# Performance work log

Hardware: AMD Instinct MI355X
Metric: run time of the kernel (lower is better)

Reference implementation:

```python
import jax
import jax.numpy as jnp
from jax import lax
import numpy as np

INPUT_SIZE = 2
COND_SIZE = 4
HIDDEN = 128
LATENT = 32
DEC_IN = INPUT_SIZE + LATENT + COND_SIZE + 1  # 39
DT = 0.05


def setup_inputs() -> dict:
    key = jax.random.key(0)
    ks = jax.random.split(key, 9)
    B = 8192
    s = 1.0 / np.sqrt(HIDDEN)  # PyTorch LSTM init scale
    z = jax.random.normal(ks[0], (B, LATENT), jnp.float32)
    condition = jax.random.normal(ks[1], (B, COND_SIZE), jnp.float32)
    start_point = jax.random.normal(ks[2], (B, INPUT_SIZE), jnp.float32)
    W_ih = jax.random.uniform(ks[3], (4 * HIDDEN, DEC_IN), jnp.float32, -s, s)
    W_hh = jax.random.uniform(ks[4], (4 * HIDDEN, HIDDEN), jnp.float32, -s, s)
    b_ih = jax.random.uniform(ks[5], (4 * HIDDEN,), jnp.float32, -s, s)
    b_hh = jax.random.uniform(ks[6], (4 * HIDDEN,), jnp.float32, -s, s)
    W_out = jax.random.uniform(ks[7], (INPUT_SIZE, HIDDEN), jnp.float32, -s, s)
    b_out = jax.random.uniform(ks[8], (INPUT_SIZE,), jnp.float32, -s, s)
    return {
        "z": z, "condition": condition, "start_point": start_point,
        "W_ih": W_ih, "W_hh": W_hh, "b_ih": b_ih, "b_hh": b_hh,
        "W_out": W_out, "b_out": b_out, "seq_len": 2048,
    }


def reference(z, condition, start_point, W_ih, W_hh, b_ih, b_hh, W_out, b_out, seq_len):
    B = z.shape[0]
    dt = jnp.full((B, 1), DT, dtype=z.dtype)  # constant delta_t per step
    # precompute the static part of the per-step input projection: [z, cond, dt]
    # columns of W_ih: [x(2) | z(32) | cond(4) | dt(1)]
    static_in = jnp.concatenate([z, condition, dt], axis=-1)  # [B, 37]
    static_proj = static_in @ W_ih[:, INPUT_SIZE:].T + b_ih + b_hh  # [B, 4H]
    W_ih_x = W_ih[:, :INPUT_SIZE]  # [4H, 2]

    def step(carry, _):
        x_t, h, c = carry
        gates = x_t @ W_ih_x.T + static_proj + h @ W_hh.T  # [B, 4H]
        i, f, g, o = jnp.split(gates, 4, axis=-1)
        i = jax.nn.sigmoid(i)
        f = jax.nn.sigmoid(f)
        g = jnp.tanh(g)
        o = jax.nn.sigmoid(o)
        c = f * c + i * g
        h = o * jnp.tanh(c)
        x_next = h @ W_out.T + b_out  # [B, input_size]
        return (x_next, h, c), x_next

    h0 = jnp.zeros((B, HIDDEN), z.dtype)
    c0 = jnp.zeros((B, HIDDEN), z.dtype)
    _, ys = lax.scan(step, (start_point, h0, c0), None, length=seq_len)
    return jnp.transpose(ys, (1, 0, 2))  # [B, seq_len, input_size]
```

## Files before the change

### kernel.cpp

```cpp
#include <hip/hip_runtime.h>

typedef short bf16x8 __attribute__((ext_vector_type(8)));
typedef float f32x4 __attribute__((ext_vector_type(4)));

#define LOG2E 1.44269504088896340736f

__device__ __forceinline__ unsigned short f2bf(float x) {
    unsigned u = __builtin_bit_cast(unsigned, x);
    return (unsigned short)((u + 0x7fffu + ((u >> 16) & 1u)) >> 16);
}

__global__ __launch_bounds__(512, 4)
void lstm_persist(const float* __restrict__ zP, const float* __restrict__ condP,
                  const float* __restrict__ startP, const float* __restrict__ WihP,
                  const float* __restrict__ WhhP, const float* __restrict__ bihP,
                  const float* __restrict__ bhhP, const float* __restrict__ WoutP,
                  const float* __restrict__ boutP, float* __restrict__ outP)
{
    __shared__ unsigned short hist[8 * 16 * 128];
    char* const lds = (char*)hist;

    const int tid  = threadIdx.x;
    const int wave = tid >> 6;
    const int lane = tid & 63;
    const int lo   = lane & 15;
    const int gq   = lane >> 4;
    const int r0   = blockIdx.x * 16;
    const int hid0 = wave * 16;

    const float K2 = 2.0f * LOG2E;
    const float ss[4] = { -LOG2E, -LOG2E, 2.0f * LOG2E, -LOG2E };

    float wxs0[4], wxs1[4], bias[4];
    bf16x8 bfrag[4][4];
    #pragma unroll
    for (int s = 0; s < 4; ++s) {
        const int col = s * 128 + hid0 + lo;
        const float wx0 = WihP[col * 39 + 0];
        const float wx1 = WihP[col * 39 + 1];
        wxs0[s] = ss[s] * wx0;
        wxs1[s] = ss[s] * wx1;
        bias[s] = bihP[col] + bhhP[col];
        #pragma unroll
        for (int kt = 0; kt < 4; ++kt) {
            bf16x8 f;
            #pragma unroll
            for (int j = 0; j < 8; ++j) {
                const int k = kt * 32 + gq * 8 + j;
                const float w = WhhP[col * 128 + k]
                              + wx0 * WoutP[k] + wx1 * WoutP[128 + k];
                f[j] = (short)f2bf(ss[s] * w);
            }
            bfrag[s][kt] = f;
        }
    }

    bf16x8 wof[4];
    #pragma unroll
    for (int kt = 0; kt < 4; ++kt) {
        bf16x8 f;
        #pragma unroll
        for (int j = 0; j < 8; ++j) {
            const int k = kt * 32 + gq * 8 + j;
            f[j] = (lo < 2) ? (short)f2bf(WoutP[lo * 128 + k]) : (short)0;
        }
        wof[kt] = f;
    }
    const float bo = (lo < 2) ? boutP[lo] : 0.0f;

    f32x4 sp[4];
    #pragma unroll
    for (int s = 0; s < 4; ++s)
        #pragma unroll
        for (int rr = 0; rr < 4; ++rr)
            sp[s][rr] = bias[s];

    for (int j = 0; j < 32; ++j) {
        float w[4];
        #pragma unroll
        for (int s = 0; s < 4; ++s) w[s] = WihP[(s * 128 + hid0 + lo) * 39 + 2 + j];
        #pragma unroll
        for (int rr = 0; rr < 4; ++rr) {
            const int row = r0 + gq * 4 + rr;
            const float si = zP[row * 32 + j];
            #pragma unroll
            for (int s = 0; s < 4; ++s) sp[s][rr] += si * w[s];
        }
    }
    for (int j = 0; j < 4; ++j) {
        float w[4];
        #pragma unroll
        for (int s = 0; s < 4; ++s) w[s] = WihP[(s * 128 + hid0 + lo) * 39 + 34 + j];
        #pragma unroll
        for (int rr = 0; rr < 4; ++rr) {
            const int row = r0 + gq * 4 + rr;
            const float si = condP[row * 4 + j];
            #pragma unroll
            for (int s = 0; s < 4; ++s) sp[s][rr] += si * w[s];
        }
    }
    #pragma unroll
    for (int s = 0; s < 4; ++s) {
        const float w = 0.05f * WihP[(s * 128 + hid0 + lo) * 39 + 38];
        #pragma unroll
        for (int rr = 0; rr < 4; ++rr) sp[s][rr] = ss[s] * (sp[s][rr] + w);
    }

    int wroff[4];
    #pragma unroll
    for (int rr = 0; rr < 4; ++rr) {
        const int row = gq * 4 + rr;
        wroff[rr] = (row * 256 + (hid0 + lo) * 2) ^ ((row & 7) << 4);
    }
    int rdoff[4];
    #pragma unroll
    for (int kt = 0; kt < 4; ++kt)
        rdoff[kt] = (lo * 256 + kt * 64 + gq * 16) ^ ((lo & 7) << 4);

    f32x4 cst = f32x4{0.f, 0.f, 0.f, 0.f};

    auto tail = [&](f32x4 (&acc)[4], const int wbase) {
        float h[4];
        #pragma unroll
        for (int rr = 0; rr < 4; ++rr) {
            const float si = __builtin_amdgcn_rcpf(1.0f + __builtin_amdgcn_exp2f(acc[0][rr]));
            const float sf = __builtin_amdgcn_rcpf(1.0f + __builtin_amdgcn_exp2f(acc[1][rr]));
            const float rg = __builtin_amdgcn_rcpf(1.0f + __builtin_amdgcn_exp2f(acc[2][rr]));
            const float so = __builtin_amdgcn_rcpf(1.0f + __builtin_amdgcn_exp2f(acc[3][rr]));
            const float tg = __builtin_fmaf(rg, -2.0f, 1.0f);
            const float cn = __builtin_fmaf(sf, cst[rr], si * tg);
            cst[rr] = cn;
            const float rc = __builtin_amdgcn_rcpf(1.0f + __builtin_amdgcn_exp2f(cn * K2));
            const float tc = __builtin_fmaf(rc, -2.0f, 1.0f);
            h[rr] = so * tc;
        }
        unsigned p01, p23;
        asm("v_cvt_pk_bf16_f32 %0, %1, %2" : "=v"(p01) : "v"(h[0]), "v"(h[1]));
        asm("v_cvt_pk_bf16_f32 %0, %1, %2" : "=v"(p23) : "v"(h[2]), "v"(h[3]));
        *(unsigned short*)(lds + wbase + wroff[0]) = (unsigned short)(p01 & 0xffffu);
        *(unsigned short*)(lds + wbase + wroff[1]) = (unsigned short)(p01 >> 16);
        *(unsigned short*)(lds + wbase + wroff[2]) = (unsigned short)(p23 & 0xffffu);
        *(unsigned short*)(lds + wbase + wroff[3]) = (unsigned short)(p23 >> 16);
    };

    {
        f32x4 acc0[4];
        #pragma unroll
        for (int s = 0; s < 4; ++s) acc0[s] = sp[s];
        #pragma unroll
        for (int rr = 0; rr < 4; ++rr) {
            const int row = r0 + gq * 4 + rr;
            const float x0 = startP[row * 2 + 0];
            const float x1 = startP[row * 2 + 1];
            #pragma unroll
            for (int s = 0; s < 4; ++s)
                acc0[s][rr] += x0 * wxs0[s] + x1 * wxs1[s];
        }
        tail(acc0, 0);
    }
    #pragma unroll
    for (int s = 0; s < 4; ++s) {
        const float bx = wxs0[s] * boutP[0] + wxs1[s] * boutP[1];
        #pragma unroll
        for (int rr = 0; rr < 4; ++rr) sp[s][rr] += bx;
    }
    __syncthreads();

    #pragma unroll 1
    for (int t = 1; t < 2048; ++t) {
        const int rbase = ((t - 1) & 7) * 4096;
        const int wbase = (t & 7) * 4096;

        bf16x8 af[4];
        #pragma unroll
        for (int kt = 0; kt < 4; ++kt)
            af[kt] = __builtin_bit_cast(bf16x8, *(const f32x4*)(lds + rbase + rdoff[kt]));

        f32x4 acc[4];
        #pragma unroll
        for (int s = 0; s < 4; ++s) {
            f32x4 a = sp[s];
            #pragma unroll
            for (int kt = 0; kt < 4; ++kt)
                a = __builtin_amdgcn_mfma_f32_16x16x32_bf16(af[kt], bfrag[s][kt], a, 0, 0, 0);
            acc[s] = a;
        }
        tail(acc, wbase);
        __syncthreads();

        if ((t & 7) == 7) {
            f32x4 xacc = f32x4{0.f, 0.f, 0.f, 0.f};
            #pragma unroll
            for (int kt = 0; kt < 4; ++kt) {
                const bf16x8 a = __builtin_bit_cast(bf16x8,
                    *(const f32x4*)(lds + wave * 4096 + rdoff[kt]));
                xacc = __builtin_amdgcn_mfma_f32_16x16x32_bf16(a, wof[kt], xacc, 0, 0, 0);
            }
            const int tg = t - 7 + wave;
            if (lo < 2) {
                #pragma unroll
                for (int rr = 0; rr < 4; ++rr) {
                    const int row = gq * 4 + rr;
                    outP[(size_t)(r0 + row) * 4096 + tg * 2 + lo] = xacc[rr] + bo;
                }
            }
            __syncthreads();
        }
    }
}

extern "C" void kernel_launch(void* const* d_in, const int* in_sizes, int n_in,
                              void* d_out, int out_size, void* d_ws, size_t ws_size,
                              hipStream_t stream) {
    const float* z    = (const float*)d_in[0];
    const float* cond = (const float*)d_in[1];
    const float* strt = (const float*)d_in[2];
    const float* Wih  = (const float*)d_in[3];
    const float* Whh  = (const float*)d_in[4];
    const float* bih  = (const float*)d_in[5];
    const float* bhh  = (const float*)d_in[6];
    const float* Wout = (const float*)d_in[7];
    const float* bout = (const float*)d_in[8];
    float* out = (float*)d_out;

    hipLaunchKernelGGL(lstm_persist, dim3(512), dim3(512), 0, stream,
                       z, cond, strt, Wih, Whh, bih, bhh, Wout, bout, out);
}
```

Before: 3.130 ms.

## Double LDS history ring, drop extra barrier, merge gate reciprocals, stagger blocks

```diff
diff --git a/kernel.cpp b/kernel.cpp
--- a/kernel.cpp
+++ b/kernel.cpp
@@ -17,7 +17,7 @@
                   const float* __restrict__ bhhP, const float* __restrict__ WoutP,
                   const float* __restrict__ boutP, float* __restrict__ outP)
 {
-    __shared__ unsigned short hist[8 * 16 * 128];
+    __shared__ unsigned short hist[16 * 16 * 128];
     char* const lds = (char*)hist;
 
     const int tid  = threadIdx.x;
@@ -123,16 +123,20 @@
         float h[4];
         #pragma unroll
         for (int rr = 0; rr < 4; ++rr) {
-            const float si = __builtin_amdgcn_rcpf(1.0f + __builtin_amdgcn_exp2f(acc[0][rr]));
-            const float sf = __builtin_amdgcn_rcpf(1.0f + __builtin_amdgcn_exp2f(acc[1][rr]));
-            const float rg = __builtin_amdgcn_rcpf(1.0f + __builtin_amdgcn_exp2f(acc[2][rr]));
-            const float so = __builtin_amdgcn_rcpf(1.0f + __builtin_amdgcn_exp2f(acc[3][rr]));
-            const float tg = __builtin_fmaf(rg, -2.0f, 1.0f);
-            const float cn = __builtin_fmaf(sf, cst[rr], si * tg);
+            const float yi = __builtin_amdgcn_exp2f(__builtin_fminf(acc[0][rr], 40.f));
+            const float yf = __builtin_amdgcn_exp2f(__builtin_fminf(acc[1][rr], 40.f));
+            const float yg = __builtin_amdgcn_exp2f(__builtin_fminf(acc[2][rr], 40.f));
+            const float yo = __builtin_amdgcn_exp2f(__builtin_fminf(acc[3][rr], 40.f));
+            const float pf  = 1.0f + yf;
+            const float pig = (1.0f + yi) * (1.0f + yg);
+            const float r3  = __builtin_amdgcn_rcpf(pf * pig);
+            const float sf  = pig * r3;
+            const float ig  = (yg - 1.0f) * pf * r3;
+            const float cn  = __builtin_fmaf(sf, cst[rr], ig);
             cst[rr] = cn;
-            const float rc = __builtin_amdgcn_rcpf(1.0f + __builtin_amdgcn_exp2f(cn * K2));
-            const float tc = __builtin_fmaf(rc, -2.0f, 1.0f);
-            h[rr] = so * tc;
+            const float yc  = __builtin_amdgcn_exp2f(__builtin_fminf(cn * K2, 40.f));
+            const float roc = __builtin_amdgcn_rcpf((1.0f + yo) * (1.0f + yc));
+            h[rr] = (yc - 1.0f) * roc;
         }
         unsigned p01, p23;
         asm("v_cvt_pk_bf16_f32 %0, %1, %2" : "=v"(p01) : "v"(h[0]), "v"(h[1]));
@@ -166,37 +170,25 @@
     }
     __syncthreads();
 
+    if (blockIdx.x & 1) {
+        asm volatile("s_sleep 7\n s_sleep 7\n s_sleep 7\n s_sleep 7\n s_sleep 7");
+    }
+
     #pragma unroll 1
     for (int t = 1; t < 2048; ++t) {
-        const int rbase = ((t - 1) & 7) * 4096;
-        const int wbase = (t & 7) * 4096;
-
-        bf16x8 af[4];
-        #pragma unroll
-        for (int kt = 0; kt < 4; ++kt)
-            af[kt] = __builtin_bit_cast(bf16x8, *(const f32x4*)(lds + rbase + rdoff[kt]));
-
-        f32x4 acc[4];
-        #pragma unroll
-        for (int s = 0; s < 4; ++s) {
-            f32x4 a = sp[s];
-            #pragma unroll
-            for (int kt = 0; kt < 4; ++kt)
-                a = __builtin_amdgcn_mfma_f32_16x16x32_bf16(af[kt], bfrag[s][kt], a, 0, 0, 0);
-            acc[s] = a;
-        }
-        tail(acc, wbase);
-        __syncthreads();
-
-        if ((t & 7) == 7) {
+        const int rbase = ((t - 1) & 15) * 4096;
+        const int wbase = (t & 15) * 4096;
+
+        if ((t & 7) == 0) {
+            const int sbase = (wave + ((t - 8) & 15)) * 4096;
             f32x4 xacc = f32x4{0.f, 0.f, 0.f, 0.f};
             #pragma unroll
             for (int kt = 0; kt < 4; ++kt) {
                 const bf16x8 a = __builtin_bit_cast(bf16x8,
-                    *(const f32x4*)(lds + wave * 4096 + rdoff[kt]));
+                    *(const f32x4*)(lds + sbase + rdoff[kt]));
                 xacc = __builtin_amdgcn_mfma_f32_16x16x32_bf16(a, wof[kt], xacc, 0, 0, 0);
             }
-            const int tg = t - 7 + wave;
+            const int tg = t - 8 + wave;
             if (lo < 2) {
                 #pragma unroll
                 for (int rr = 0; rr < 4; ++rr) {
@@ -204,7 +196,42 @@
                     outP[(size_t)(r0 + row) * 4096 + tg * 2 + lo] = xacc[rr] + bo;
                 }
             }
-            __syncthreads();
+        }
+
+        bf16x8 af[4];
+        #pragma unroll
+        for (int kt = 0; kt < 4; ++kt)
+            af[kt] = __builtin_bit_cast(bf16x8, *(const f32x4*)(lds + rbase + rdoff[kt]));
+
+        f32x4 acc[4];
+        #pragma unroll
+        for (int s = 0; s < 4; ++s) {
+            f32x4 a = sp[s];
+            #pragma unroll
+            for (int kt = 0; kt < 4; ++kt)
+                a = __builtin_amdgcn_mfma_f32_16x16x32_bf16(af[kt], bfrag[s][kt], a, 0, 0, 0);
+            acc[s] = a;
+        }
+        tail(acc, wbase);
+        __syncthreads();
+    }
+
+    {
+        const int sbase = (wave + 8) * 4096;
+        f32x4 xacc = f32x4{0.f, 0.f, 0.f, 0.f};
+        #pragma unroll
+        for (int kt = 0; kt < 4; ++kt) {
+            const bf16x8 a = __builtin_bit_cast(bf16x8,
+                *(const f32x4*)(lds + sbase + rdoff[kt]));
+            xacc = __builtin_amdgcn_mfma_f32_16x16x32_bf16(a, wof[kt], xacc, 0, 0, 0);
+        }
+        const int tg = 2040 + wave;
+        if (lo < 2) {
+            #pragma unroll
+            for (int rr = 0; rr < 4; ++rr) {
+                const int row = gq * 4 + rr;
+                outP[(size_t)(r0 + row) * 4096 + tg * 2 + lo] = xacc[rr] + bo;
+            }
         }
     }
 }
```

Result: slower. 3.725 ms (+19.0%).

## Process two 16-row batch tiles per block to reuse weight fragments

Applied to the files above, without the earlier changes.

```diff
diff --git a/kernel.cpp b/kernel.cpp
--- a/kernel.cpp
+++ b/kernel.cpp
@@ -10,14 +10,14 @@
     return (unsigned short)((u + 0x7fffu + ((u >> 16) & 1u)) >> 16);
 }
 
-__global__ __launch_bounds__(512, 4)
+__global__ __launch_bounds__(512, 2)
 void lstm_persist(const float* __restrict__ zP, const float* __restrict__ condP,
                   const float* __restrict__ startP, const float* __restrict__ WihP,
                   const float* __restrict__ WhhP, const float* __restrict__ bihP,
                   const float* __restrict__ bhhP, const float* __restrict__ WoutP,
                   const float* __restrict__ boutP, float* __restrict__ outP)
 {
-    __shared__ unsigned short hist[8 * 16 * 128];
+    __shared__ unsigned short hist[2 * 8 * 16 * 128];
     char* const lds = (char*)hist;
 
     const int tid  = threadIdx.x;
@@ -25,7 +25,7 @@
     const int lane = tid & 63;
     const int lo   = lane & 15;
     const int gq   = lane >> 4;
-    const int r0   = blockIdx.x * 16;
+    const int r0   = blockIdx.x * 32;
     const int hid0 = wave * 16;
 
     const float K2 = 2.0f * LOG2E;
@@ -68,12 +68,11 @@
     }
     const float bo = (lo < 2) ? boutP[lo] : 0.0f;
 
-    f32x4 sp[4];
+    f32x4 spA[4], spB[4];
     #pragma unroll
     for (int s = 0; s < 4; ++s)
         #pragma unroll
-        for (int rr = 0; rr < 4; ++rr)
-            sp[s][rr] = bias[s];
+        for (int rr = 0; rr < 4; ++rr) { spA[s][rr] = bias[s]; spB[s][rr] = bias[s]; }
 
     for (int j = 0; j < 32; ++j) {
         float w[4];
@@ -81,10 +80,11 @@
         for (int s = 0; s < 4; ++s) w[s] = WihP[(s * 128 + hid0 + lo) * 39 + 2 + j];
         #pragma unroll
         for (int rr = 0; rr < 4; ++rr) {
-            const int row = r0 + gq * 4 + rr;
-            const float si = zP[row * 32 + j];
-            #pragma unroll
-            for (int s = 0; s < 4; ++s) sp[s][rr] += si * w[s];
+            const int rowA = r0 + gq * 4 + rr;
+            const float sa = zP[rowA * 32 + j];
+            const float sb = zP[(rowA + 16) * 32 + j];
+            #pragma unroll
+            for (int s = 0; s < 4; ++s) { spA[s][rr] += sa * w[s]; spB[s][rr] += sb * w[s]; }
         }
     }
     for (int j = 0; j < 4; ++j) {
@@ -93,17 +93,21 @@
         for (int s = 0; s < 4; ++s) w[s] = WihP[(s * 128 + hid0 + lo) * 39 + 34 + j];
         #pragma unroll
         for (int rr = 0; rr < 4; ++rr) {
-            const int row = r0 + gq * 4 + rr;
-            const float si = condP[row * 4 + j];
-            #pragma unroll
-            for (int s = 0; s < 4; ++s) sp[s][rr] += si * w[s];
+            const int rowA = r0 + gq * 4 + rr;
+            const float sa = condP[rowA * 4 + j];
+            const float sb = condP[(rowA + 16) * 4 + j];
+            #pragma unroll
+            for (int s = 0; s < 4; ++s) { spA[s][rr] += sa * w[s]; spB[s][rr] += sb * w[s]; }
         }
     }
     #pragma unroll
     for (int s = 0; s < 4; ++s) {
         const float w = 0.05f * WihP[(s * 128 + hid0 + lo) * 39 + 38];
         #pragma unroll
-        for (int rr = 0; rr < 4; ++rr) sp[s][rr] = ss[s] * (sp[s][rr] + w);
+        for (int rr = 0; rr < 4; ++rr) {
+            spA[s][rr] = ss[s] * (spA[s][rr] + w);
+            spB[s][rr] = ss[s] * (spB[s][rr] + w);
+        }
     }
 
     int wroff[4];
@@ -117,9 +121,10 @@
     for (int kt = 0; kt < 4; ++kt)
         rdoff[kt] = (lo * 256 + kt * 64 + gq * 16) ^ ((lo & 7) << 4);
 
-    f32x4 cst = f32x4{0.f, 0.f, 0.f, 0.f};
-
-    auto tail = [&](f32x4 (&acc)[4], const int wbase) {
+    f32x4 cstA = f32x4{0.f, 0.f, 0.f, 0.f};
+    f32x4 cstB = f32x4{0.f, 0.f, 0.f, 0.f};
+
+    auto tail = [&](f32x4 (&acc)[4], f32x4& cst, const int wbyte) {
         float h[4];
         #pragma unroll
         for (int rr = 0; rr < 4; ++rr) {
@@ -137,32 +142,37 @@
         unsigned p01, p23;
         asm("v_cvt_pk_bf16_f32 %0, %1, %2" : "=v"(p01) : "v"(h[0]), "v"(h[1]));
         asm("v_cvt_pk_bf16_f32 %0, %1, %2" : "=v"(p23) : "v"(h[2]), "v"(h[3]));
-        *(unsigned short*)(lds + wbase + wroff[0]) = (unsigned short)(p01 & 0xffffu);
-        *(unsigned short*)(lds + wbase + wroff[1]) = (unsigned short)(p01 >> 16);
-        *(unsigned short*)(lds + wbase + wroff[2]) = (unsigned short)(p23 & 0xffffu);
-        *(unsigned short*)(lds + wbase + wroff[3]) = (unsigned short)(p23 >> 16);
+        *(unsigned short*)(lds + wbyte + wroff[0]) = (unsigned short)(p01 & 0xffffu);
+        *(unsigned short*)(lds + wbyte + wroff[1]) = (unsigned short)(p01 >> 16);
+        *(unsigned short*)(lds + wbyte + wroff[2]) = (unsigned short)(p23 & 0xffffu);
+        *(unsigned short*)(lds + wbyte + wroff[3]) = (unsigned short)(p23 >> 16);
     };
 
     {
-        f32x4 acc0[4];
-        #pragma unroll
-        for (int s = 0; s < 4; ++s) acc0[s] = sp[s];
-        #pragma unroll
-        for (int rr = 0; rr < 4; ++rr) {
-            const int row = r0 + gq * 4 + rr;
-            const float x0 = startP[row * 2 + 0];
-            const float x1 = startP[row * 2 + 1];
-            #pragma unroll
-            for (int s = 0; s < 4; ++s)
-                acc0[s][rr] += x0 * wxs0[s] + x1 * wxs1[s];
-        }
-        tail(acc0, 0);
+        f32x4 accA[4], accB[4];
+        #pragma unroll
+        for (int s = 0; s < 4; ++s) { accA[s] = spA[s]; accB[s] = spB[s]; }
+        #pragma unroll
+        for (int rr = 0; rr < 4; ++rr) {
+            const int rowA = r0 + gq * 4 + rr;
+            const float a0 = startP[rowA * 2 + 0];
+            const float a1 = startP[rowA * 2 + 1];
+            const float b0 = startP[(rowA + 16) * 2 + 0];
+            const float b1 = startP[(rowA + 16) * 2 + 1];
+            #pragma unroll
+            for (int s = 0; s < 4; ++s) {
+                accA[s][rr] += a0 * wxs0[s] + a1 * wxs1[s];
+                accB[s][rr] += b0 * wxs0[s] + b1 * wxs1[s];
+            }
+        }
+        tail(accA, cstA, 0);
+        tail(accB, cstB, 32768);
     }
     #pragma unroll
     for (int s = 0; s < 4; ++s) {
         const float bx = wxs0[s] * boutP[0] + wxs1[s] * boutP[1];
         #pragma unroll
-        for (int rr = 0; rr < 4; ++rr) sp[s][rr] += bx;
+        for (int rr = 0; rr < 4; ++rr) { spA[s][rr] += bx; spB[s][rr] += bx; }
     }
     __syncthreads();
 
@@ -171,37 +181,57 @@
         const int rbase = ((t - 1) & 7) * 4096;
         const int wbase = (t & 7) * 4096;
 
-        bf16x8 af[4];
+        bf16x8 afA[4];
         #pragma unroll
         for (int kt = 0; kt < 4; ++kt)
-            af[kt] = __builtin_bit_cast(bf16x8, *(const f32x4*)(lds + rbase + rdoff[kt]));
-
-        f32x4 acc[4];
+            afA[kt] = __builtin_bit_cast(bf16x8, *(const f32x4*)(lds + rbase + rdoff[kt]));
+        f32x4 accA[4];
         #pragma unroll
         for (int s = 0; s < 4; ++s) {
-            f32x4 a = sp[s];
+            f32x4 a = spA[s];
             #pragma unroll
             for (int kt = 0; kt < 4; ++kt)
-                a = __builtin_amdgcn_mfma_f32_16x16x32_bf16(af[kt], bfrag[s][kt], a, 0, 0, 0);
-            acc[s] = a;
-        }
-        tail(acc, wbase);
+                a = __builtin_amdgcn_mfma_f32_16x16x32_bf16(afA[kt], bfrag[s][kt], a, 0, 0, 0);
+            accA[s] = a;
+        }
+
+        bf16x8 afB[4];
+        #pragma unroll
+        for (int kt = 0; kt < 4; ++kt)
+            afB[kt] = __builtin_bit_cast(bf16x8, *(const f32x4*)(lds + 32768 + rbase + rdoff[kt]));
+        f32x4 accB[4];
+        #pragma unroll
+        for (int s = 0; s < 4; ++s) {
+            f32x4 a = spB[s];
+            #pragma unroll
+            for (int kt = 0; kt < 4; ++kt)
+                a = __builtin_amdgcn_mfma_f32_16x16x32_bf16(afB[kt], bfrag[s][kt], a, 0, 0, 0);
+            accB[s] = a;
+        }
+
+        tail(accA, cstA, wbase);
+        tail(accB, cstB, 32768 + wbase);
         __syncthreads();
 
         if ((t & 7) == 7) {
-            f32x4 xacc = f32x4{0.f, 0.f, 0.f, 0.f};
+            f32x4 xa = f32x4{0.f, 0.f, 0.f, 0.f};
+            f32x4 xb = f32x4{0.f, 0.f, 0.f, 0.f};
             #pragma unroll
             for (int kt = 0; kt < 4; ++kt) {
                 const bf16x8 a = __builtin_bit_cast(bf16x8,
                     *(const f32x4*)(lds + wave * 4096 + rdoff[kt]));
-                xacc = __builtin_amdgcn_mfma_f32_16x16x32_bf16(a, wof[kt], xacc, 0, 0, 0);
+                xa = __builtin_amdgcn_mfma_f32_16x16x32_bf16(a, wof[kt], xa, 0, 0, 0);
+                const bf16x8 b = __builtin_bit_cast(bf16x8,
+                    *(const f32x4*)(lds + 32768 + wave * 4096 + rdoff[kt]));
+                xb = __builtin_amdgcn_mfma_f32_16x16x32_bf16(b, wof[kt], xb, 0, 0, 0);
             }
             const int tg = t - 7 + wave;
             if (lo < 2) {
                 #pragma unroll
                 for (int rr = 0; rr < 4; ++rr) {
                     const int row = gq * 4 + rr;
-                    outP[(size_t)(r0 + row) * 4096 + tg * 2 + lo] = xacc[rr] + bo;
+                    outP[(size_t)(r0 + row) * 4096 + tg * 2 + lo] = xa[rr] + bo;
+                    outP[(size_t)(r0 + 16 + row) * 4096 + tg * 2 + lo] = xb[rr] + bo;
                 }
             }
             __syncthreads();
@@ -223,6 +253,6 @@
     const float* bout = (const float*)d_in[8];
     float* out = (float*)d_out;
 
-    hipLaunchKernelGGL(lstm_persist, dim3(512), dim3(512), 0, stream,
+    hipLaunchKernelGGL(lstm_persist, dim3(256), dim3(512), 0, stream,
                        z, cond, strt, Wih, Whh, bih, bhh, Wout, bout, out);
 }
```

New measurement: 2.903 ms. -7.3%, faster.

## Split waves into MFMA producers and activation consumers with two interleaved row groups

Applied to the files above, without the earlier changes.

```diff
diff --git a/kernel.cpp b/kernel.cpp
--- a/kernel.cpp
+++ b/kernel.cpp
@@ -10,203 +10,273 @@
     return (unsigned short)((u + 0x7fffu + ((u >> 16) & 1u)) >> 16);
 }
 
-__global__ __launch_bounds__(512, 4)
+__global__ __launch_bounds__(1024, 4)
 void lstm_persist(const float* __restrict__ zP, const float* __restrict__ condP,
                   const float* __restrict__ startP, const float* __restrict__ WihP,
                   const float* __restrict__ WhhP, const float* __restrict__ bihP,
                   const float* __restrict__ bhhP, const float* __restrict__ WoutP,
                   const float* __restrict__ boutP, float* __restrict__ outP)
 {
-    __shared__ unsigned short hist[8 * 16 * 128];
-    char* const lds = (char*)hist;
+    __shared__ __align__(16) char lds[151552];
 
     const int tid  = threadIdx.x;
     const int wave = tid >> 6;
     const int lane = tid & 63;
     const int lo   = lane & 15;
     const int gq   = lane >> 4;
-    const int r0   = blockIdx.x * 16;
-    const int hid0 = wave * 16;
-
+    const int r0   = blockIdx.x * 32;
+    const int role = (wave >> 2) & 1;
+    const int ridx = (wave & 3) | ((wave >> 3) << 2);
+
+    const float ss[4] = { -LOG2E, -LOG2E, 2.0f * LOG2E, -LOG2E };
     const float K2 = 2.0f * LOG2E;
-    const float ss[4] = { -LOG2E, -LOG2E, 2.0f * LOG2E, -LOG2E };
-
-    float wxs0[4], wxs1[4], bias[4];
-    bf16x8 bfrag[4][4];
-    #pragma unroll
-    for (int s = 0; s < 4; ++s) {
-        const int col = s * 128 + hid0 + lo;
-        const float wx0 = WihP[col * 39 + 0];
-        const float wx1 = WihP[col * 39 + 1];
-        wxs0[s] = ss[s] * wx0;
-        wxs1[s] = ss[s] * wx1;
-        bias[s] = bihP[col] + bhhP[col];
-        #pragma unroll
-        for (int kt = 0; kt < 4; ++kt) {
-            bf16x8 f;
-            #pragma unroll
-            for (int j = 0; j < 8; ++j) {
-                const int k = kt * 32 + gq * 8 + j;
-                const float w = WhhP[col * 128 + k]
-                              + wx0 * WoutP[k] + wx1 * WoutP[128 + k];
-                f[j] = (short)f2bf(ss[s] * w);
-            }
-            bfrag[s][kt] = f;
-        }
-    }
-
-    bf16x8 wof[4];
-    #pragma unroll
-    for (int kt = 0; kt < 4; ++kt) {
-        bf16x8 f;
-        #pragma unroll
-        for (int j = 0; j < 8; ++j) {
-            const int k = kt * 32 + gq * 8 + j;
-            f[j] = (lo < 2) ? (short)f2bf(WoutP[lo * 128 + k]) : (short)0;
-        }
-        wof[kt] = f;
-    }
-    const float bo = (lo < 2) ? boutP[lo] : 0.0f;
-
-    f32x4 sp[4];
-    #pragma unroll
-    for (int s = 0; s < 4; ++s)
-        #pragma unroll
-        for (int rr = 0; rr < 4; ++rr)
-            sp[s][rr] = bias[s];
-
-    for (int j = 0; j < 32; ++j) {
-        float w[4];
-        #pragma unroll
-        for (int s = 0; s < 4; ++s) w[s] = WihP[(s * 128 + hid0 + lo) * 39 + 2 + j];
-        #pragma unroll
-        for (int rr = 0; rr < 4; ++rr) {
-            const int row = r0 + gq * 4 + rr;
-            const float si = zP[row * 32 + j];
-            #pragma unroll
-            for (int s = 0; s < 4; ++s) sp[s][rr] += si * w[s];
-        }
-    }
-    for (int j = 0; j < 4; ++j) {
-        float w[4];
-        #pragma unroll
-        for (int s = 0; s < 4; ++s) w[s] = WihP[(s * 128 + hid0 + lo) * 39 + 34 + j];
-        #pragma unroll
-        for (int rr = 0; rr < 4; ++rr) {
-            const int row = r0 + gq * 4 + rr;
-            const float si = condP[row * 4 + j];
-            #pragma unroll
-            for (int s = 0; s < 4; ++s) sp[s][rr] += si * w[s];
-        }
-    }
-    #pragma unroll
-    for (int s = 0; s < 4; ++s) {
-        const float w = 0.05f * WihP[(s * 128 + hid0 + lo) * 39 + 38];
-        #pragma unroll
-        for (int rr = 0; rr < 4; ++rr) sp[s][rr] = ss[s] * (sp[s][rr] + w);
-    }
-
-    int wroff[4];
-    #pragma unroll
-    for (int rr = 0; rr < 4; ++rr) {
-        const int row = gq * 4 + rr;
-        wroff[rr] = (row * 256 + (hid0 + lo) * 2) ^ ((row & 7) << 4);
-    }
+
+    constexpr int GBUF  = 40960;
+    constexpr int HB    = 81920;
+    constexpr int HRING = 32768;
+    constexpr int WOFB  = 147456;
+
     int rdoff[4];
     #pragma unroll
     for (int kt = 0; kt < 4; ++kt)
         rdoff[kt] = (lo * 256 + kt * 64 + gq * 16) ^ ((lo & 7) << 4);
 
-    f32x4 cst = f32x4{0.f, 0.f, 0.f, 0.f};
-
-    auto tail = [&](f32x4 (&acc)[4], const int wbase) {
+    if (role == 0) {
+        const int hid0 = ridx * 16;
+        bf16x8 bfrag[4][4];
+        #pragma unroll
+        for (int s = 0; s < 4; ++s) {
+            const int col = s * 128 + hid0 + lo;
+            const float wx0 = WihP[col * 39 + 0];
+            const float wx1 = WihP[col * 39 + 1];
+            #pragma unroll
+            for (int kt = 0; kt < 4; ++kt) {
+                bf16x8 f;
+                #pragma unroll
+                for (int j = 0; j < 8; ++j) {
+                    const int k = kt * 32 + gq * 8 + j;
+                    const float w = WhhP[col * 128 + k]
+                                  + wx0 * WoutP[k] + wx1 * WoutP[128 + k];
+                    f[j] = (short)f2bf(ss[s] * w);
+                }
+                bfrag[s][kt] = f;
+            }
+        }
+        int gwoff[4];
+        #pragma unroll
+        for (int s = 0; s < 4; ++s)
+            gwoff[s] = (s * 128 + hid0 + lo) * 80 + gq * 16;
+
+        __syncthreads();
+
+        #pragma unroll 1
+        for (int t = 1; t < 2048; ++t) {
+            const int sb = ((t - 1) & 7) * 4096;
+            {
+                const char* hb = lds + HB + sb;
+                bf16x8 af[4];
+                #pragma unroll
+                for (int kt = 0; kt < 4; ++kt)
+                    af[kt] = __builtin_bit_cast(bf16x8, *(const f32x4*)(hb + rdoff[kt]));
+                #pragma unroll
+                for (int s = 0; s < 4; ++s) {
+                    f32x4 a = f32x4{0.f, 0.f, 0.f, 0.f};
+                    #pragma unroll
+                    for (int kt = 0; kt < 4; ++kt)
+                        a = __builtin_amdgcn_mfma_f32_16x16x32_bf16(af[kt], bfrag[s][kt], a, 0, 0, 0);
+                    *(f32x4*)(lds + gwoff[s]) = a;
+                }
+            }
+            __syncthreads();
+            {
+                const char* hb = lds + HB + HRING + sb;
+                bf16x8 af[4];
+                #pragma unroll
+                for (int kt = 0; kt < 4; ++kt)
+                    af[kt] = __builtin_bit_cast(bf16x8, *(const f32x4*)(hb + rdoff[kt]));
+                #pragma unroll
+                for (int s = 0; s < 4; ++s) {
+                    f32x4 a = f32x4{0.f, 0.f, 0.f, 0.f};
+                    #pragma unroll
+                    for (int kt = 0; kt < 4; ++kt)
+                        a = __builtin_amdgcn_mfma_f32_16x16x32_bf16(af[kt], bfrag[s][kt], a, 0, 0, 0);
+                    *(f32x4*)(lds + GBUF + gwoff[s]) = a;
+                }
+            }
+            __syncthreads();
+        }
+        __syncthreads();
+        return;
+    }
+
+    const int hcol = ridx * 16 + lo;
+    int groff[4], wroff[4];
+    #pragma unroll
+    for (int s = 0; s < 4; ++s)
+        groff[s] = (s * 128 + hcol) * 80 + gq * 16;
+    #pragma unroll
+    for (int i = 0; i < 4; ++i) {
+        const int row = gq * 4 + i;
+        wroff[i] = (row * 256 + hcol * 2) ^ ((row & 7) << 4);
+    }
+    const float bo = (lo < 2) ? boutP[lo] : 0.0f;
+
+    f32x4 spA[4], spB[4];
+    float wxs0[4], wxs1[4];
+    {
+        float w38[4];
+        #pragma unroll
+        for (int s = 0; s < 4; ++s) {
+            const int col = s * 128 + hcol;
+            const float b = bihP[col] + bhhP[col];
+            wxs0[s] = ss[s] * WihP[col * 39 + 0];
+            wxs1[s] = ss[s] * WihP[col * 39 + 1];
+            w38[s]  = WihP[col * 39 + 38];
+            #pragma unroll
+            for (int i = 0; i < 4; ++i) { spA[s][i] = b; spB[s][i] = b; }
+        }
+        for (int j = 0; j < 32; ++j) {
+            float w[4];
+            #pragma unroll
+            for (int s = 0; s < 4; ++s) w[s] = WihP[(s * 128 + hcol) * 39 + 2 + j];
+            #pragma unroll
+            for (int i = 0; i < 4; ++i) {
+                const int rowA = r0 + gq * 4 + i;
+                const float za = zP[rowA * 32 + j];
+                const float zb = zP[(rowA + 16) * 32 + j];
+                #pragma unroll
+                for (int s = 0; s < 4; ++s) { spA[s][i] += za * w[s]; spB[s][i] += zb * w[s]; }
+            }
+        }
+        for (int j = 0; j < 4; ++j) {
+            float w[4];
+            #pragma unroll
+            for (int s = 0; s < 4; ++s) w[s] = WihP[(s * 128 + hcol) * 39 + 34 + j];
+            #pragma unroll
+            for (int i = 0; i < 4; ++i) {
+                const int rowA = r0 + gq * 4 + i;
+                const float ca = condP[rowA * 4 + j];
+                const float cb = condP[(rowA + 16) * 4 + j];
+                #pragma unroll
+                for (int s = 0; s < 4; ++s) { spA[s][i] += ca * w[s]; spB[s][i] += cb * w[s]; }
+            }
+        }
+        #pragma unroll
+        for (int s = 0; s < 4; ++s)
+            #pragma unroll
+            for (int i = 0; i < 4; ++i) {
+                spA[s][i] = ss[s] * (spA[s][i] + 0.05f * w38[s]);
+                spB[s][i] = ss[s] * (spB[s][i] + 0.05f * w38[s]);
+            }
+    }
+
+    f32x4 cstA = f32x4{0.f, 0.f, 0.f, 0.f};
+    f32x4 cstB = f32x4{0.f, 0.f, 0.f, 0.f};
+
+    auto tailcore = [&](f32x4 (&g4)[4], f32x4& c, const int hbase) {
         float h[4];
         #pragma unroll
-        for (int rr = 0; rr < 4; ++rr) {
-            const float si = __builtin_amdgcn_rcpf(1.0f + __builtin_amdgcn_exp2f(acc[0][rr]));
-            const float sf = __builtin_amdgcn_rcpf(1.0f + __builtin_amdgcn_exp2f(acc[1][rr]));
-            const float rg = __builtin_amdgcn_rcpf(1.0f + __builtin_amdgcn_exp2f(acc[2][rr]));
-            const float so = __builtin_amdgcn_rcpf(1.0f + __builtin_amdgcn_exp2f(acc[3][rr]));
+        for (int i = 0; i < 4; ++i) {
+            const float si = __builtin_amdgcn_rcpf(1.0f + __builtin_amdgcn_exp2f(g4[0][i]));
+            const float sf = __builtin_amdgcn_rcpf(1.0f + __builtin_amdgcn_exp2f(g4[1][i]));
+            const float rg = __builtin_amdgcn_rcpf(1.0f + __builtin_amdgcn_exp2f(g4[2][i]));
+            const float so = __builtin_amdgcn_rcpf(1.0f + __builtin_amdgcn_exp2f(g4[3][i]));
             const float tg = __builtin_fmaf(rg, -2.0f, 1.0f);
-            const float cn = __builtin_fmaf(sf, cst[rr], si * tg);
-            cst[rr] = cn;
+            const float cn = __builtin_fmaf(sf, c[i], si * tg);
+            c[i] = cn;
             const float rc = __builtin_amdgcn_rcpf(1.0f + __builtin_amdgcn_exp2f(cn * K2));
             const float tc = __builtin_fmaf(rc, -2.0f, 1.0f);
-            h[rr] = so * tc;
+            h[i] = so * tc;
         }
         unsigned p01, p23;
         asm("v_cvt_pk_bf16_f32 %0, %1, %2" : "=v"(p01) : "v"(h[0]), "v"(h[1]));
         asm("v_cvt_pk_bf16_f32 %0, %1, %2" : "=v"(p23) : "v"(h[2]), "v"(h[3]));
-        *(unsigned short*)(lds + wbase + wroff[0]) = (unsigned short)(p01 & 0xffffu);
-        *(unsigned short*)(lds + wbase + wroff[1]) = (unsigned short)(p01 >> 16);
-        *(unsigned short*)(lds + wbase + wroff[2]) = (unsigned short)(p23 & 0xffffu);
-        *(unsigned short*)(lds + wbase + wroff[3]) = (unsigned short)(p23 >> 16);
+        *(unsigned short*)(lds + hbase + wroff[0]) = (unsigned short)(p01 & 0xffffu);
+        *(unsigned short*)(lds + hbase + wroff[1]) = (unsigned short)(p01 >> 16);
+        *(unsigned short*)(lds + hbase + wroff[2]) = (unsigned short)(p23 & 0xffffu);
+        *(unsigned short*)(lds + hbase + wroff[3]) = (unsigned short)(p23 >> 16);
     };
+    auto dotail = [&](const int gbase, const f32x4 (&spg)[4], f32x4& c, const int hbase) {
+        f32x4 g4[4];
+        #pragma unroll
+        for (int s = 0; s < 4; ++s)
+            g4[s] = *(const f32x4*)(lds + gbase + groff[s]) + spg[s];
+        tailcore(g4, c, hbase);
+    };
+    auto dooutg = [&](const int X, const int tb) {
+        const char* hb = lds + HB + X * HRING + ridx * 4096;
+        f32x4 x = f32x4{0.f, 0.f, 0.f, 0.f};
+        #pragma unroll
+        for (int kt = 0; kt < 4; ++kt) {
+            const bf16x8 a = __builtin_bit_cast(bf16x8, *(const f32x4*)(hb + rdoff[kt]));
+            const bf16x8 w = __builtin_bit_cast(bf16x8, *(const f32x4*)(lds + WOFB + kt * 1024 + lane * 16));
+            x = __builtin_amdgcn_mfma_f32_16x16x32_bf16(a, w, x, 0, 0, 0);
+        }
+        const int tg = tb + ridx;
+        if (lo < 2) {
+            #pragma unroll
+            for (int rr = 0; rr < 4; ++rr)
+                outP[(size_t)(r0 + X * 16 + gq * 4 + rr) * 4096 + tg * 2 + lo] = x[rr] + bo;
+        }
+    };
+
+    if (ridx == 0) {
+        #pragma unroll
+        for (int kt = 0; kt < 4; ++kt) {
+            bf16x8 f;
+            #pragma unroll
+            for (int j = 0; j < 8; ++j) {
+                const int k = kt * 32 + gq * 8 + j;
+                f[j] = (lo < 2) ? (short)f2bf(WoutP[lo * 128 + k]) : (short)0;
+            }
+            *(bf16x8*)(lds + WOFB + kt * 1024 + lane * 16) = f;
+        }
+    }
 
     {
-        f32x4 acc0[4];
-        #pragma unroll
-        for (int s = 0; s < 4; ++s) acc0[s] = sp[s];
-        #pragma unroll
-        for (int rr = 0; rr < 4; ++rr) {
-            const int row = r0 + gq * 4 + rr;
-            const float x0 = startP[row * 2 + 0];
-            const float x1 = startP[row * 2 + 1];
-            #pragma unroll
-            for (int s = 0; s < 4; ++s)
-                acc0[s][rr] += x0 * wxs0[s] + x1 * wxs1[s];
-        }
-        tail(acc0, 0);
+        f32x4 a0[4], b0[4];
+        #pragma unroll
+        for (int s = 0; s < 4; ++s) { a0[s] = spA[s]; b0[s] = spB[s]; }
+        #pragma unroll
+        for (int i = 0; i < 4; ++i) {
+            const int rowA = r0 + gq * 4 + i;
+            const float xa0 = startP[rowA * 2 + 0];
+            const float xa1 = startP[rowA * 2 + 1];
+            const float xb0 = startP[(rowA + 16) * 2 + 0];
+            const float xb1 = startP[(rowA + 16) * 2 + 1];
+            #pragma unroll
+            for (int s = 0; s < 4; ++s) {
+                a0[s][i] += xa0 * wxs0[s] + xa1 * wxs1[s];
+                b0[s][i] += xb0 * wxs0[s] + xb1 * wxs1[s];
+            }
+        }
+        tailcore(a0, cstA, HB + 0);
+        tailcore(b0, cstB, HB + HRING + 0);
     }
     #pragma unroll
     for (int s = 0; s < 4; ++s) {
         const float bx = wxs0[s] * boutP[0] + wxs1[s] * boutP[1];
         #pragma unroll
-        for (int rr = 0; rr < 4; ++rr) sp[s][rr] += bx;
+        for (int i = 0; i < 4; ++i) { spA[s][i] += bx; spB[s][i] += bx; }
     }
     __syncthreads();
 
     #pragma unroll 1
     for (int t = 1; t < 2048; ++t) {
-        const int rbase = ((t - 1) & 7) * 4096;
-        const int wbase = (t & 7) * 4096;
-
-        bf16x8 af[4];
-        #pragma unroll
-        for (int kt = 0; kt < 4; ++kt)
-            af[kt] = __builtin_bit_cast(bf16x8, *(const f32x4*)(lds + rbase + rdoff[kt]));
-
-        f32x4 acc[4];
-        #pragma unroll
-        for (int s = 0; s < 4; ++s) {
-            f32x4 a = sp[s];
-            #pragma unroll
-            for (int kt = 0; kt < 4; ++kt)
-                a = __builtin_amdgcn_mfma_f32_16x16x32_bf16(af[kt], bfrag[s][kt], a, 0, 0, 0);
-            acc[s] = a;
-        }
-        tail(acc, wbase);
-        __syncthreads();
-
-        if ((t & 7) == 7) {
-            f32x4 xacc = f32x4{0.f, 0.f, 0.f, 0.f};
-            #pragma unroll
-            for (int kt = 0; kt < 4; ++kt) {
-                const bf16x8 a = __builtin_bit_cast(bf16x8,
-                    *(const f32x4*)(lds + wave * 4096 + rdoff[kt]));
-                xacc = __builtin_amdgcn_mfma_f32_16x16x32_bf16(a, wof[kt], xacc, 0, 0, 0);
-            }
-            const int tg = t - 7 + wave;
-            if (lo < 2) {
-                #pragma unroll
-                for (int rr = 0; rr < 4; ++rr) {
-                    const int row = gq * 4 + rr;
-                    outP[(size_t)(r0 + row) * 4096 + tg * 2 + lo] = xacc[rr] + bo;
-                }
-            }
-            __syncthreads();
-        }
-    }
+        const int sb = ((t - 1) & 7) * 4096;
+        if (t > 1)
+            dotail(GBUF, spB, cstB, HB + HRING + sb);
+        if ((t & 7) == 0) dooutg(0, t - 8);
+        __syncthreads();
+        dotail(0, spA, cstA, HB + (t & 7) * 4096);
+        if ((t & 7) == 0) dooutg(1, t - 8);
+        __syncthreads();
+    }
+
+    dotail(GBUF, spB, cstB, HB + HRING + 7 * 4096);
+    __syncthreads();
+    dooutg(0, 2040);
+    dooutg(1, 2040);
 }
 
 extern "C" void kernel_launch(void* const* d_in, const int* in_sizes, int n_in,
@@ -223,6 +293,6 @@
     const float* bout = (const float*)d_in[8];
     float* out = (float*)d_out;
 
-    hipLaunchKernelGGL(lstm_persist, dim3(512), dim3(512), 0, stream,
+    hipLaunchKernelGGL(lstm_persist, dim3(256), dim3(1024), 0, stream,
                        z, cond, strt, Wih, Whh, bih, bhh, Wout, bout, out);
 }
```

New measurement: 3.527 ms. 1.13x slower.
